# Kernel tuning notes

Hardware: AMD Instinct MI355X
Metric: run time of the kernel (lower is better)

Reference implementation:

```python
import jax, jax.numpy as jnp
import numpy as np
from jax import lax

WIN = 11
SIGMA = 1.5


def _gaussian_kernel2d(win_size, channels, dtype):
    g = jnp.arange(win_size, dtype=dtype) - win_size // 2
    g = jnp.exp(-(g ** 2) / (2.0 * SIGMA ** 2))
    g = g / g.sum()
    k2 = jnp.einsum('i,j->ij', g, g)
    return jnp.broadcast_to(k2, (channels, 1, win_size, win_size))


def setup_inputs() -> dict:
    key = jax.random.key(0)
    k1, k2 = jax.random.split(key)
    B, C, H, W = 8, 19, 512, 512
    pred = jax.random.normal(k1, (B, C, H, W), dtype=jnp.float32)
    target = jax.random.randint(k2, (B, H, W), 0, C, dtype=jnp.int64)
    return {"pred": pred, "target": target}


def reference(pred, target):
    B, C, H, W = pred.shape
    win = min(H, W, WIN)
    p = jax.nn.softmax(pred, axis=1)
    t = jax.nn.one_hot(target, C, dtype=p.dtype).transpose(0, 3, 1, 2)  # [B,C,H,W]
    kernel = _gaussian_kernel2d(win, C, p.dtype)

    def dwconv(x):  # depthwise valid conv over all classes at once
        return lax.conv_general_dilated(x, kernel, (1, 1), 'VALID',
                                        feature_group_count=C)

    mu1 = dwconv(p)
    mu2 = dwconv(t)
    mu12 = mu1 * mu2
    mu1sq = mu1 * mu1
    mu2sq = mu2 * mu2
    var1 = dwconv(p * p) - mu1sq
    var2 = dwconv(t * t) - mu2sq
    covar = dwconv(p * t) - mu12

    L = 1.0
    c1 = (0.01 * L) ** 2
    c2 = (0.03 * L) ** 2
    cs = (2.0 * covar + c2) / (var1 + var2 + c2)
    ss = (2.0 * mu12 + c1) / (mu1sq + mu2sq + c1) * cs  # [B,C,H',W']

    ss = ss.reshape(B, C, -1).mean(axis=-1)  # per (batch, class) SSIM
    ss = jax.nn.relu(ss)  # nonnegative=True
    # loss = mean over classes of (1 - mean over batch of ss) == 1 - mean(ss)
    return 1.0 - ss.mean()
```

## Files before the change

### kernel.cpp

```cpp
#include <hip/hip_runtime.h>

namespace {

constexpr int B = 8, C = 19, H = 512, W = 512;
constexpr int OH = 502, OW = 502;
constexpr int HW = H * W;

constexpr int TH = 32;
constexpr int TW = 54;
constexpr int RPT = 8;
constexpr int NJ = RPT + 10;
constexpr int LW = 68;

__device__ constexpr float G[11] = {
    0.00102838f, 0.00759876f, 0.03600077f, 0.10936070f, 0.21300553f,
    0.26601173f,
    0.21300553f, 0.10936070f, 0.03600077f, 0.00759876f, 0.00102838f};

__global__ __launch_bounds__(256) void denom_kernel(
    const float* __restrict__ pred, const int* __restrict__ target,
    float* __restrict__ rs, unsigned char* __restrict__ t8,
    float* __restrict__ accum) {
  int tid = blockIdx.x * 256 + threadIdx.x;
  if (blockIdx.x == 0 && threadIdx.x < B * C) accum[threadIdx.x] = 0.0f;
  int p4 = tid * 4;
  int b = p4 / HW;
  int px = p4 - b * HW;
  const float4* pp = (const float4*)(pred + (size_t)b * C * HW + px);
  float4 s = {0.f, 0.f, 0.f, 0.f};
#pragma unroll
  for (int c = 0; c < C; ++c) {
    float4 v = pp[c * (HW / 4)];
    s.x += __expf(v.x);
    s.y += __expf(v.y);
    s.z += __expf(v.z);
    s.w += __expf(v.w);
  }
  float4 r;
  r.x = 1.0f / s.x;
  r.y = 1.0f / s.y;
  r.z = 1.0f / s.z;
  r.w = 1.0f / s.w;
  ((float4*)rs)[tid] = r;
  int4 t = ((const int4*)target)[tid];
  uchar4 tc;
  tc.x = (unsigned char)t.x;
  tc.y = (unsigned char)t.y;
  tc.z = (unsigned char)t.z;
  tc.w = (unsigned char)t.w;
  ((uchar4*)t8)[tid] = tc;
}

__global__ __launch_bounds__(256, 4) void ssim_kernel(
    const float* __restrict__ pred, const float* __restrict__ rs,
    const unsigned char* __restrict__ t8, float* __restrict__ accum) {
  __shared__ float vOut[4][TH][LW];

  const int tid = threadIdx.x;
  const int x0 = blockIdx.x * TW;
  const int y0 = blockIdx.y * TH;
  const int z = blockIdx.z;
  const int b = z >> 2;
  const int c0 = (z & 3) * 5;
  const int c1 = min(c0 + 5, C);
  const int ow = min(TW, OW - x0);
  const int oh = min(TH, OH - y0);

  const int col = tid & 63;
  const int rg = tid >> 6;
  const int gc = min(x0 + col, W - 1);
  const int rbase = y0 + rg * RPT;

  const int prow = tid >> 3;
  const int cg = tid & 7;
  const int cbase = cg * 7;

  const float* rsb = rs + b * HW;
  const unsigned char* tb = t8 + b * HW;

  for (int c = c0; c < c1; ++c) {
    __syncthreads();

    const float* pc = pred + (size_t)(b * C + c) * HW;
    float aP[RPT] = {}, aP2[RPT] = {}, aPT[RPT] = {}, aT[RPT] = {};
#pragma unroll
    for (int j = 0; j < NJ; ++j) {
      int r = min(rbase + j, H - 1);
      int o = r * W + gc;
      float p = __expf(pc[o]) * rsb[o];
      float p2 = p * p;
      bool hit = ((int)tb[o] == c);
      float tf = hit ? 1.0f : 0.0f;
      float pt = hit ? p : 0.0f;
#pragma unroll
      for (int oo = 0; oo < RPT; ++oo) {
        int g = j - oo;
        if (g >= 0 && g < 11) {
          float gw = G[g];
          aP[oo] = fmaf(gw, p, aP[oo]);
          aP2[oo] = fmaf(gw, p2, aP2[oo]);
          aPT[oo] = fmaf(gw, pt, aPT[oo]);
          aT[oo] = fmaf(gw, tf, aT[oo]);
        }
      }
    }
#pragma unroll
    for (int oo = 0; oo < RPT; ++oo) {
      int r = rg * RPT + oo;
      vOut[0][r][col] = aP[oo];
      vOut[1][r][col] = aP2[oo];
      vOut[2][r][col] = aPT[oo];
      vOut[3][r][col] = aT[oo];
    }
    __syncthreads();

    float mres[4][7];
#pragma unroll
    for (int f = 0; f < 4; ++f) {
      float vin[17];
#pragma unroll
      for (int k = 0; k < 17; ++k) vin[k] = vOut[f][prow][cbase + k];
#pragma unroll
      for (int oo = 0; oo < 7; ++oo) {
        float s = 0.0f;
#pragma unroll
        for (int j = 0; j < 11; ++j) s = fmaf(G[j], vin[oo + j], s);
        mres[f][oo] = s;
      }
    }

    float acc = 0.0f;
    if (prow < oh) {
#pragma unroll
      for (int oo = 0; oo < 7; ++oo) {
        if (cbase + oo < ow) {
          float mu1 = mres[0][oo];
          float dp2 = mres[1][oo];
          float dpt = mres[2][oo];
          float mu2 = mres[3][oo];
          float mu1sq = mu1 * mu1;
          float mu2sq = mu2 * mu2;
          float mu12 = mu1 * mu2;
          float var1 = dp2 - mu1sq;
          float var2 = mu2 - mu2sq;
          float covar = dpt - mu12;
          const float c1c = 1e-4f, c2c = 9e-4f;
          float num = (2.0f * mu12 + c1c) * (2.0f * covar + c2c);
          float den = (mu1sq + mu2sq + c1c) * (var1 + var2 + c2c);
          acc += __fdividef(num, den);
        }
      }
    }

    for (int o2 = 32; o2 > 0; o2 >>= 1) acc += __shfl_down(acc, o2);
    if ((tid & 63) == 0) atomicAdd(&accum[b * C + c], acc);
  }
}

__global__ __launch_bounds__(256) void finish_kernel(
    const float* __restrict__ accum, float* __restrict__ out) {
  __shared__ float red[4];
  int tid = threadIdx.x;
  float v = 0.0f;
  if (tid < B * C) {
    float m = accum[tid] * (1.0f / (float)(OH * OW));
    v = m > 0.0f ? m : 0.0f;
  }
  for (int off = 32; off > 0; off >>= 1) v += __shfl_down(v, off);
  if ((tid & 63) == 0) red[tid >> 6] = v;
  __syncthreads();
  if (tid == 0)
    out[0] = 1.0f - (red[0] + red[1] + red[2] + red[3]) / (float)(B * C);
}

}

extern "C" void kernel_launch(void* const* d_in, const int* in_sizes, int n_in,
                              void* d_out, int out_size, void* d_ws,
                              size_t ws_size, hipStream_t stream) {
  const float* pred = (const float*)d_in[0];
  const int* target = (const int*)d_in[1];
  float* out = (float*)d_out;

  float* rs = (float*)d_ws;
  unsigned char* t8 = (unsigned char*)d_ws + (size_t)B * HW * sizeof(float);
  float* accum = (float*)((char*)d_ws + (size_t)B * HW * 5);

  denom_kernel<<<B * HW / 1024, 256, 0, stream>>>(pred, target, rs, t8, accum);
  dim3 grid((OW + TW - 1) / TW, (OH + TH - 1) / TH, B * 4);
  ssim_kernel<<<grid, 256, 0, stream>>>(pred, rs, t8, accum);
  finish_kernel<<<1, 256, 0, stream>>>(accum, out);
}
```

Before: 792.7 us.

## Precompute fp16 softmax and stage tiles in LDS with class bitmask

A new first kernel computes the full softmax and writes it to workspace as fp16, so the SSIM kernel no longer recomputes exp and reciprocal-sum for every halo row. The SSIM kernel stages the target as per-pixel class bitmasks and the probability tile in shared memory, and prefetches the next class tile into registers while the current one is processed. Vertical partial sums are packed as half2 to halve LDS traffic. In exchange it writes and rereads an fp16 copy of all probabilities and loses precision in the intermediates. The old fp32 path is kept as a fallback when the workspace is too small.

```diff
diff --git a/kernel.cpp b/kernel.cpp
--- a/kernel.cpp
+++ b/kernel.cpp
@@ -1,21 +1,212 @@
 #include <hip/hip_runtime.h>
+#include <hip/hip_fp16.h>
 
 namespace {
 
-constexpr int B = 8, C = 19, H = 512, W = 512;
+constexpr int B = 8, C = 19, H = 512, W = 512, HW = H * W;
 constexpr int OH = 502, OW = 502;
-constexpr int HW = H * W;
-
-constexpr int TH = 32;
-constexpr int TW = 54;
-constexpr int RPT = 8;
-constexpr int NJ = RPT + 10;
-constexpr int LW = 68;
+constexpr int TH = 32, TW = 54;
+constexpr int IH = 42, IW = 64;
+constexpr int LW = 76;
 
 __device__ constexpr float G[11] = {
     0.00102838f, 0.00759876f, 0.03600077f, 0.10936070f, 0.21300553f,
     0.26601173f,
     0.21300553f, 0.10936070f, 0.03600077f, 0.00759876f, 0.00102838f};
+
+
+__global__ __launch_bounds__(256, 4) void softmax_kernel(
+    const float* __restrict__ pred, __half* __restrict__ pH,
+    float* __restrict__ accum) {
+  const int tid = blockIdx.x * 256 + threadIdx.x;
+  if (blockIdx.x == 0 && threadIdx.x < B * C) accum[threadIdx.x] = 0.0f;
+  const int p4 = tid * 4;
+  const int b = p4 / HW;
+  const int px = p4 - b * HW;
+  const float* base = pred + (size_t)b * C * HW + px;
+  uint2 eh[C];
+  float sx = 0.f, sy = 0.f, sz = 0.f, sw = 0.f;
+#pragma unroll
+  for (int c = 0; c < C; ++c) {
+    float4 v = *(const float4*)(base + (size_t)c * HW);
+    float ex = __expf(v.x), ey = __expf(v.y);
+    float ez = __expf(v.z), ew = __expf(v.w);
+    sx += ex; sy += ey; sz += ez; sw += ew;
+    __half2 l = __floats2half2_rn(ex, ey);
+    __half2 h = __floats2half2_rn(ez, ew);
+    eh[c].x = *(const unsigned*)&l;
+    eh[c].y = *(const unsigned*)&h;
+  }
+  const float rx = 1.f / sx, ry = 1.f / sy, rz = 1.f / sz, rw = 1.f / sw;
+  __half* outb = pH + (size_t)b * C * HW + px;
+#pragma unroll
+  for (int c = 0; c < C; ++c) {
+    __half2 l = *(const __half2*)&eh[c].x;
+    __half2 h = *(const __half2*)&eh[c].y;
+    __half2 pl = __floats2half2_rn(__low2float(l) * rx, __high2float(l) * ry);
+    __half2 ph = __floats2half2_rn(__low2float(h) * rz, __high2float(h) * rw);
+    uint2 o;
+    o.x = *(const unsigned*)&pl;
+    o.y = *(const unsigned*)&ph;
+    *(uint2*)(outb + (size_t)c * HW) = o;
+  }
+}
+
+__global__ __launch_bounds__(256, 4) void ssim_kernel(
+    const __half* __restrict__ pH, const int* __restrict__ target,
+    float* __restrict__ accum) {
+  __shared__ unsigned pTu[IH * IW / 2];
+  __shared__ unsigned tmask[IH * IW];
+  __shared__ unsigned vOutU[2][TH][LW];
+  const int tid = threadIdx.x;
+  const int x0 = blockIdx.x * TW;
+  const int y0 = blockIdx.y * TH;
+  const int z = blockIdx.z;
+  const int b = z >> 2;
+  const int c0 = (z & 3) * 5;
+  const int c1 = min(c0 + 5, C);
+  const int ow = min(TW, OW - x0);
+  const int oh = min(TH, OH - y0);
+
+  const int col = tid & 63;
+  const int rg = tid >> 6;
+  const int rb = rg * 8;
+  const int prow = tid >> 3;
+  const int cg = tid & 7;
+  const int cbase = cg * 8;
+
+  {
+    const int* tb = target + b * HW;
+    for (int w = tid; w < IH * IW; w += 256) {
+      int r = w >> 6, cc = w & 63;
+      int t = tb[min(y0 + r, H - 1) * W + min(x0 + cc, W - 1)];
+      tmask[w] = 1u << t;
+    }
+  }
+  {
+    const __half* pb = pH + (size_t)(b * C + c0) * HW;
+#pragma unroll
+    for (int k = 0; k < 6; ++k) {
+      int w = tid + k * 256;
+      if (w < IH * IW / 2) {
+        int r = w >> 5, cw = w & 31;
+        pTu[w] = *(const unsigned*)(pb + min(y0 + r, H - 1) * W +
+                                    min(x0 + 2 * cw, W - 2));
+      }
+    }
+  }
+
+  float* accp = accum + b * C;
+  for (int c = c0; c < c1; ++c) {
+    __syncthreads();
+
+    if (rb < oh) {
+      float aP[8] = {}, aP2[8] = {}, aPT[8] = {}, aT[8] = {};
+#pragma unroll
+      for (int j = 0; j < 18; ++j) {
+        int lr = rb + j;
+        float pv = __half2float(((const __half*)pTu)[lr * IW + col]);
+        unsigned m = tmask[lr * IW + col];
+        float tf = (float)((m >> c) & 1u);
+        float p2 = pv * pv;
+        float pt = tf * pv;
+#pragma unroll
+        for (int oo = 0; oo < 8; ++oo) {
+          int g = j - oo;
+          if (g >= 0 && g < 11) {
+            float gw = G[g];
+            aP[oo] = fmaf(gw, pv, aP[oo]);
+            aP2[oo] = fmaf(gw, p2, aP2[oo]);
+            aPT[oo] = fmaf(gw, pt, aPT[oo]);
+            aT[oo] = fmaf(gw, tf, aT[oo]);
+          }
+        }
+      }
+#pragma unroll
+      for (int oo = 0; oo < 8; ++oo) {
+        int r = rb + oo;
+        __half2 a = __floats2half2_rn(aP[oo], aP2[oo]);
+        __half2 bb = __floats2half2_rn(aPT[oo], aT[oo]);
+        vOutU[0][r][col] = *(const unsigned*)&a;
+        vOutU[1][r][col] = *(const unsigned*)&bb;
+      }
+    }
+    __syncthreads();
+
+    const bool more = (c + 1) < c1;
+    unsigned R2[6];
+    if (more) {
+      const __half* pn = pH + (size_t)(b * C + c + 1) * HW;
+#pragma unroll
+      for (int k = 0; k < 6; ++k) {
+        int w = tid + k * 256;
+        unsigned v = 0;
+        if (w < IH * IW / 2) {
+          int r = w >> 5, cw = w & 31;
+          v = *(const unsigned*)(pn + min(y0 + r, H - 1) * W +
+                                 min(x0 + 2 * cw, W - 2));
+        }
+        R2[k] = v;
+      }
+    }
+
+    float acc = 0.0f;
+    if (rb < oh) {
+      float mu1[8] = {}, dp2[8] = {}, dpt[8] = {}, mu2[8] = {};
+#pragma unroll
+      for (int gsel = 0; gsel < 2; ++gsel) {
+        unsigned vin[18];
+#pragma unroll
+        for (int k = 0; k < 18; ++k) vin[k] = vOutU[gsel][prow][cbase + k];
+#pragma unroll
+        for (int j = 0; j < 18; ++j) {
+          __half2 hv = *(const __half2*)&vin[j];
+          float lo = __low2float(hv), hi = __high2float(hv);
+#pragma unroll
+          for (int oo = 0; oo < 8; ++oo) {
+            int g = j - oo;
+            if (g >= 0 && g < 11) {
+              float gw = G[g];
+              if (gsel == 0) {
+                mu1[oo] = fmaf(gw, lo, mu1[oo]);
+                dp2[oo] = fmaf(gw, hi, dp2[oo]);
+              } else {
+                dpt[oo] = fmaf(gw, lo, dpt[oo]);
+                mu2[oo] = fmaf(gw, hi, mu2[oo]);
+              }
+            }
+          }
+        }
+      }
+      if (prow < oh) {
+#pragma unroll
+        for (int oo = 0; oo < 8; ++oo) {
+          if (cbase + oo < ow) {
+            float m1 = mu1[oo], m2 = mu2[oo];
+            float m1s = m1 * m1, m2s = m2 * m2, m12 = m1 * m2;
+            float v1 = dp2[oo] - m1s;
+            float v2 = m2 - m2s;
+            float cv = dpt[oo] - m12;
+            float num = (2.f * m12 + 1e-4f) * (2.f * cv + 9e-4f);
+            float den = (m1s + m2s + 1e-4f) * (v1 + v2 + 9e-4f);
+            acc += __fdividef(num, den);
+          }
+        }
+      }
+      for (int o2 = 32; o2 > 0; o2 >>= 1) acc += __shfl_down(acc, o2);
+      if ((tid & 63) == 0) atomicAdd(accp + c, acc);
+    }
+
+    if (more) {
+#pragma unroll
+      for (int k = 0; k < 6; ++k) {
+        int w = tid + k * 256;
+        if (w < IH * IW / 2) pTu[w] = R2[k];
+      }
+    }
+  }
+}
+
 
 __global__ __launch_bounds__(256) void denom_kernel(
     const float* __restrict__ pred, const int* __restrict__ target,
@@ -37,25 +228,19 @@
     s.w += __expf(v.w);
   }
   float4 r;
-  r.x = 1.0f / s.x;
-  r.y = 1.0f / s.y;
-  r.z = 1.0f / s.z;
-  r.w = 1.0f / s.w;
+  r.x = 1.0f / s.x; r.y = 1.0f / s.y; r.z = 1.0f / s.z; r.w = 1.0f / s.w;
   ((float4*)rs)[tid] = r;
   int4 t = ((const int4*)target)[tid];
   uchar4 tc;
-  tc.x = (unsigned char)t.x;
-  tc.y = (unsigned char)t.y;
-  tc.z = (unsigned char)t.z;
-  tc.w = (unsigned char)t.w;
+  tc.x = (unsigned char)t.x; tc.y = (unsigned char)t.y;
+  tc.z = (unsigned char)t.z; tc.w = (unsigned char)t.w;
   ((uchar4*)t8)[tid] = tc;
 }
 
-__global__ __launch_bounds__(256, 4) void ssim_kernel(
+__global__ __launch_bounds__(256, 4) void ssim_f32_kernel(
     const float* __restrict__ pred, const float* __restrict__ rs,
     const unsigned char* __restrict__ t8, float* __restrict__ accum) {
-  __shared__ float vOut[4][TH][LW];
-
+  __shared__ float vOut[4][TH][68];
   const int tid = threadIdx.x;
   const int x0 = blockIdx.x * TW;
   const int y0 = blockIdx.y * TH;
@@ -65,26 +250,22 @@
   const int c1 = min(c0 + 5, C);
   const int ow = min(TW, OW - x0);
   const int oh = min(TH, OH - y0);
-
   const int col = tid & 63;
   const int rg = tid >> 6;
   const int gc = min(x0 + col, W - 1);
-  const int rbase = y0 + rg * RPT;
-
+  const int rbase = y0 + rg * 8;
   const int prow = tid >> 3;
   const int cg = tid & 7;
   const int cbase = cg * 7;
-
   const float* rsb = rs + b * HW;
   const unsigned char* tb = t8 + b * HW;
 
   for (int c = c0; c < c1; ++c) {
     __syncthreads();
-
     const float* pc = pred + (size_t)(b * C + c) * HW;
-    float aP[RPT] = {}, aP2[RPT] = {}, aPT[RPT] = {}, aT[RPT] = {};
-#pragma unroll
-    for (int j = 0; j < NJ; ++j) {
+    float aP[8] = {}, aP2[8] = {}, aPT[8] = {}, aT[8] = {};
+#pragma unroll
+    for (int j = 0; j < 18; ++j) {
       int r = min(rbase + j, H - 1);
       int o = r * W + gc;
       float p = __expf(pc[o]) * rsb[o];
@@ -93,7 +274,7 @@
       float tf = hit ? 1.0f : 0.0f;
       float pt = hit ? p : 0.0f;
 #pragma unroll
-      for (int oo = 0; oo < RPT; ++oo) {
+      for (int oo = 0; oo < 8; ++oo) {
         int g = j - oo;
         if (g >= 0 && g < 11) {
           float gw = G[g];
@@ -105,8 +286,8 @@
       }
     }
 #pragma unroll
-    for (int oo = 0; oo < RPT; ++oo) {
-      int r = rg * RPT + oo;
+    for (int oo = 0; oo < 8; ++oo) {
+      int r = rg * 8 + oo;
       vOut[0][r][col] = aP[oo];
       vOut[1][r][col] = aP2[oo];
       vOut[2][r][col] = aPT[oo];
@@ -128,30 +309,22 @@
         mres[f][oo] = s;
       }
     }
-
     float acc = 0.0f;
     if (prow < oh) {
 #pragma unroll
       for (int oo = 0; oo < 7; ++oo) {
         if (cbase + oo < ow) {
-          float mu1 = mres[0][oo];
-          float dp2 = mres[1][oo];
-          float dpt = mres[2][oo];
-          float mu2 = mres[3][oo];
-          float mu1sq = mu1 * mu1;
-          float mu2sq = mu2 * mu2;
-          float mu12 = mu1 * mu2;
-          float var1 = dp2 - mu1sq;
-          float var2 = mu2 - mu2sq;
-          float covar = dpt - mu12;
-          const float c1c = 1e-4f, c2c = 9e-4f;
-          float num = (2.0f * mu12 + c1c) * (2.0f * covar + c2c);
-          float den = (mu1sq + mu2sq + c1c) * (var1 + var2 + c2c);
+          float m1 = mres[0][oo], m2 = mres[3][oo];
+          float m1s = m1 * m1, m2s = m2 * m2, m12 = m1 * m2;
+          float v1 = mres[1][oo] - m1s;
+          float v2 = m2 - m2s;
+          float cv = mres[2][oo] - m12;
+          float num = (2.f * m12 + 1e-4f) * (2.f * cv + 9e-4f);
+          float den = (m1s + m2s + 1e-4f) * (v1 + v2 + 9e-4f);
           acc += __fdividef(num, den);
         }
       }
     }
-
     for (int o2 = 32; o2 > 0; o2 >>= 1) acc += __shfl_down(acc, o2);
     if ((tid & 63) == 0) atomicAdd(&accum[b * C + c], acc);
   }
@@ -182,12 +355,22 @@
   const int* target = (const int*)d_in[1];
   float* out = (float*)d_out;
 
-  float* rs = (float*)d_ws;
-  unsigned char* t8 = (unsigned char*)d_ws + (size_t)B * HW * sizeof(float);
-  float* accum = (float*)((char*)d_ws + (size_t)B * HW * 5);
-
-  denom_kernel<<<B * HW / 1024, 256, 0, stream>>>(pred, target, rs, t8, accum);
+  const size_t needH = (size_t)B * C * HW * 2 + (size_t)B * C * 4;
   dim3 grid((OW + TW - 1) / TW, (OH + TH - 1) / TH, B * 4);
-  ssim_kernel<<<grid, 256, 0, stream>>>(pred, rs, t8, accum);
-  finish_kernel<<<1, 256, 0, stream>>>(accum, out);
-}
+
+  if (ws_size >= needH) {
+    __half* pH = (__half*)d_ws;
+    float* accum = (float*)((char*)d_ws + (size_t)B * C * HW * 2);
+    softmax_kernel<<<B * HW / 1024, 256, 0, stream>>>(pred, pH, accum);
+    ssim_kernel<<<grid, 256, 0, stream>>>(pH, target, accum);
+    finish_kernel<<<1, 256, 0, stream>>>(accum, out);
+  } else {
+    float* rs = (float*)d_ws;
+    unsigned char* t8 = (unsigned char*)d_ws + (size_t)B * HW * 4;
+    float* accum = (float*)((char*)d_ws + (size_t)B * HW * 5);
+    denom_kernel<<<B * HW / 1024, 256, 0, stream>>>(pred, target, rs, t8,
+                                                    accum);
+    ssim_f32_kernel<<<grid, 256, 0, stream>>>(pred, rs, t8, accum);
+    finish_kernel<<<1, 256, 0, stream>>>(accum, out);
+  }
+}
```

Result: faster. 774.6 us (-2.3%).
